# Performance work log

Measured on AMD Instinct MI355X. Metric: run time of the kernel, lower is better.

## Reference

```python
import jax, jax.numpy as jnp
import numpy as np
from jax import lax

B, T, F, H, D = 16384, 79, 3, 256, 256  # batch, levels, n_input_fields, rnn_channels, dense_width


def setup_inputs() -> dict:
    key = jax.random.key(0)
    ks = jax.random.split(key, 8)
    return {
        "x0": jax.random.normal(ks[0], (B, T), dtype=jnp.float32),
        "x1": jax.random.normal(ks[1], (B, T), dtype=jnp.float32),
        "x2": jax.random.normal(ks[2], (B, T), dtype=jnp.float32),
        # SimpleRNN params: kernel [F,H], recurrent kernel [H,H] (scaled small so relu recurrence stays stable), bias [H]
        "W_in": jax.random.normal(ks[3], (F, H), dtype=jnp.float32) * 0.1,
        "U": jax.random.normal(ks[4], (H, H), dtype=jnp.float32) * 0.05,
        "b_rnn": jnp.zeros((H,), dtype=jnp.float32),
        # MLPBlock depth=1: single Dense(D)
        "W_d": jax.random.normal(ks[5], (H, D), dtype=jnp.float32) * 0.05,
        "b_d": jnp.zeros((D,), dtype=jnp.float32),
    }


def reference(x0, x1, x2, W_in, U, b_rnn, W_d, b_d):
    # CombineInputs(-1, expand=True): stack fields on new trailing axis -> [B, T, F]
    x = jnp.stack([x0, x1, x2], axis=-1)
    # go_backwards=True: SimpleRNN consumes the sequence in reverse order
    x = x[:, ::-1, :]
    # Batched input projection (hoisted out of the recurrence): [B, T, H]
    xp = jnp.einsum("btf,fh->bth", x, W_in) + b_rnn
    xp_t = jnp.swapaxes(xp, 0, 1)  # [T, B, H] for scan over time

    def step(h, xt):
        h = jax.nn.relu(xt + h @ U)
        return h, None

    h0 = jnp.zeros((x.shape[0], W_in.shape[1]), dtype=x.dtype)
    hT, _ = lax.scan(step, h0, xp_t)  # final hidden state [B, H]
    # MLPBlock(depth=1, combine_inputs=False): single Dense, no activation
    return hT @ W_d + b_d
```

## Files before the change

### kernel.cpp

```cpp
#include <hip/hip_runtime.h>
#include <hip/hip_bf16.h>
#include <stdint.h>

#define Bsz   16384
#define Tt    79
#define Dd    256
#define KP    272
#define LROW  280
#define NTILE 32
#define THR   256

typedef __attribute__((ext_vector_type(8)))  short short8;
typedef __attribute__((ext_vector_type(4)))  float float4_;
typedef __attribute__((ext_vector_type(16))) float float16_;

__device__ __forceinline__ unsigned short f2bf(float f){
  unsigned u = __float_as_uint(f);
  u += 0x7fffu + ((u >> 16) & 1u);
  return (unsigned short)(u >> 16);
}
__device__ __forceinline__ unsigned pk2(float a, float b){
  __hip_bfloat162 h = __float22bfloat162_rn(make_float2(a, b));
  return *(unsigned*)&h;
}

__global__ void build_tables(const float* __restrict__ W_in,
                             const float* __restrict__ U,
                             const float* __restrict__ b_rnn,
                             const float* __restrict__ W_d,
                             const float* __restrict__ b_d,
                             unsigned short* __restrict__ Ut,
                             unsigned short* __restrict__ Wdt){
  const int TBL = 256 * KP;
  int idx = blockIdx.x * 256 + threadIdx.x;
  if (idx >= 2 * TBL) return;
  int tb  = idx / TBL;
  int rem = idx - tb * TBL;
  int m = rem / KP;
  int k = rem - m * KP;
  float v = 0.f;
  if (tb == 0){
    if      (k < 256) v = U[k * 256 + m];
    else if (k < 259) v = W_in[(k - 256) * 256 + m];
    else if (k == 259) v = b_rnn[m];
  } else {
    if      (k < 256) v = W_d[k * 256 + m];
    else if (k == 259) v = b_d[m];
  }
  unsigned short o = f2bf(v);
  if (tb == 0) Ut[rem] = o; else Wdt[rem] = o;
}

__global__ __launch_bounds__(THR, 2) void rnn_main(
    const float* __restrict__ x0,
    const float* __restrict__ x1,
    const float* __restrict__ x2,
    const unsigned short* __restrict__ Ut,
    const unsigned short* __restrict__ Wdt,
    float* __restrict__ out){
  __shared__ __align__(16) short hbuf[2][NTILE * LROW];

  const int tid  = threadIdx.x;
  const int lane = tid & 63;
  const int wm   = tid >> 6;
  const int nl   = lane & 31;
  const int hi   = lane >> 5;
  const int hi8  = hi * 8;
  const int bbase = blockIdx.x * NTILE;

  {
    int4* p = (int4*)&hbuf[0][0];
    const int tot = 2 * NTILE * LROW * 2 / 16;
    int4 z = make_int4(0, 0, 0, 0);
    for (int i = tid; i < tot; i += THR) p[i] = z;
  }
  __syncthreads();

  if (tid < NTILE){
    hbuf[0][tid * LROW + 259] = (short)0x3F80;
    hbuf[1][tid * LROW + 259] = (short)0x3F80;
  }

  const bool stager = (lane < 8);
  const int  sn  = wm * 8 + (lane & 7);
  const int  sgb = bbase + sn;
  if (stager){
    int tr = Tt - 1;
    float a = x0[sgb * Tt + tr];
    float b = x1[sgb * Tt + tr];
    float c = x2[sgb * Tt + tr];
    *(unsigned*)&hbuf[0][sn * LROW + 256] = pk2(a, b);
    hbuf[0][sn * LROW + 258] = (short)f2bf(c);
  }

  short8 afr[2][17];
  #pragma unroll
  for (int mt = 0; mt < 2; ++mt){
    const unsigned short* p = Ut + (wm * 64 + mt * 32 + nl) * KP + hi8;
    #pragma unroll
    for (int kt = 0; kt < 17; ++kt){
      afr[mt][kt] = *(const short8*)(p + kt * 16);
    }
  }

  __syncthreads();

  const float16_ zz16 = {0.f,0.f,0.f,0.f,0.f,0.f,0.f,0.f,
                         0.f,0.f,0.f,0.f,0.f,0.f,0.f,0.f};

  auto step = [&](const short* __restrict__ hb, short* __restrict__ hw, int t){
    float xa = 0.f, xb = 0.f, xc = 0.f;
    const bool pf = stager && (t < Tt - 1);
    if (pf){
      int tr = Tt - 2 - t;
      xa = x0[sgb * Tt + tr];
      xb = x1[sgb * Tt + tr];
      xc = x2[sgb * Tt + tr];
    }

    float16_ a0, a1;
    #pragma unroll
    for (int kt = 0; kt < 17; ++kt){
      short8 b = *(const short8*)&hb[nl * LROW + kt * 16 + hi8];
      if (kt == 0){
        a0 = __builtin_amdgcn_mfma_f32_32x32x16_bf16(afr[0][0], b, zz16, 0, 0, 0);
        a1 = __builtin_amdgcn_mfma_f32_32x32x16_bf16(afr[1][0], b, zz16, 0, 0, 0);
      } else {
        a0 = __builtin_amdgcn_mfma_f32_32x32x16_bf16(afr[0][kt], b, a0, 0, 0, 0);
        a1 = __builtin_amdgcn_mfma_f32_32x32x16_bf16(afr[1][kt], b, a1, 0, 0, 0);
      }
    }

    #pragma unroll
    for (int g = 0; g < 4; ++g){
      uint2 w;
      w.x = pk2(fmaxf(a0[4*g+0], 0.f), fmaxf(a0[4*g+1], 0.f));
      w.y = pk2(fmaxf(a0[4*g+2], 0.f), fmaxf(a0[4*g+3], 0.f));
      *(uint2*)&hw[nl * LROW + wm * 64 +      8 * g + 4 * hi] = w;
      w.x = pk2(fmaxf(a1[4*g+0], 0.f), fmaxf(a1[4*g+1], 0.f));
      w.y = pk2(fmaxf(a1[4*g+2], 0.f), fmaxf(a1[4*g+3], 0.f));
      *(uint2*)&hw[nl * LROW + wm * 64 + 32 + 8 * g + 4 * hi] = w;
    }
    if (pf){
      *(unsigned*)&hw[sn * LROW + 256] = pk2(xa, xb);
      hw[sn * LROW + 258] = (short)f2bf(xc);
    }
    __syncthreads();
  };

  #pragma unroll 1
  for (int t = 0; t < Tt - 1; t += 2){
    step(&hbuf[0][0], &hbuf[1][0], t);
    step(&hbuf[1][0], &hbuf[0][0], t + 1);
  }
  step(&hbuf[0][0], &hbuf[1][0], Tt - 1);

  const short* hb = &hbuf[1][0];
  float16_ o0, o1;
  #pragma unroll
  for (int kt = 0; kt < 17; ++kt){
    short8 w0 = *(const short8*)(Wdt + (wm * 64 +      nl) * KP + kt * 16 + hi8);
    short8 w1 = *(const short8*)(Wdt + (wm * 64 + 32 + nl) * KP + kt * 16 + hi8);
    short8 b  = *(const short8*)&hb[nl * LROW + kt * 16 + hi8];
    if (kt == 0){
      o0 = __builtin_amdgcn_mfma_f32_32x32x16_bf16(w0, b, zz16, 0, 0, 0);
      o1 = __builtin_amdgcn_mfma_f32_32x32x16_bf16(w1, b, zz16, 0, 0, 0);
    } else {
      o0 = __builtin_amdgcn_mfma_f32_32x32x16_bf16(w0, b, o0, 0, 0, 0);
      o1 = __builtin_amdgcn_mfma_f32_32x32x16_bf16(w1, b, o1, 0, 0, 0);
    }
  }
  #pragma unroll
  for (int g = 0; g < 4; ++g){
    int m0 = wm * 64 + 8 * g + 4 * hi;
    float4_ v0 = {o0[4*g+0], o0[4*g+1], o0[4*g+2], o0[4*g+3]};
    float4_ v1 = {o1[4*g+0], o1[4*g+1], o1[4*g+2], o1[4*g+3]};
    *(float4_*)&out[(bbase + nl) * Dd + m0]      = v0;
    *(float4_*)&out[(bbase + nl) * Dd + m0 + 32] = v1;
  }
}

extern "C" void kernel_launch(void* const* d_in, const int* in_sizes, int n_in,
                              void* d_out, int out_size, void* d_ws, size_t ws_size,
                              hipStream_t stream){
  const float* x0    = (const float*)d_in[0];
  const float* x1    = (const float*)d_in[1];
  const float* x2    = (const float*)d_in[2];
  const float* W_in  = (const float*)d_in[3];
  const float* U     = (const float*)d_in[4];
  const float* b_rnn = (const float*)d_in[5];
  const float* W_d   = (const float*)d_in[6];
  const float* b_d   = (const float*)d_in[7];

  unsigned short* Ut  = (unsigned short*)d_ws;
  unsigned short* Wdt = Ut + 256 * KP;
  float* out = (float*)d_out;

  build_tables<<<(2 * 256 * KP + 255) / 256, 256, 0, stream>>>(W_in, U, b_rnn, W_d, b_d, Ut, Wdt);
  rnn_main<<<Bsz / NTILE, THR, 0, stream>>>(x0, x1, x2, Ut, Wdt, out);
}
```

Measured before the change: 223.2 us.

## Fuse weight table build into RNN kernel and split hidden dim across 8 waves

Drops the separate table-building kernel: each wave now loads U, W_in, b_rnn, W_d and b_d straight from fp32 global memory and packs them to bf16 in registers. The block grows to 512 threads, so each of 8 waves owns 32 hidden channels instead of 64. That halves the MFMA chain per wave per timestep and the register-resident weight fragments, and the launch bound now asks for 4 blocks per CU to raise occupancy. The costs are strided uncoalesced fp32 weight loads repeated by every block, and a barrier each timestep that now spans twice as many waves.

```diff
diff --git a/kernel.cpp b/kernel.cpp
--- a/kernel.cpp
+++ b/kernel.cpp
@@ -8,55 +8,31 @@
 #define KP    272
 #define LROW  280
 #define NTILE 32
-#define THR   256
+#define THR   512
 
 typedef __attribute__((ext_vector_type(8)))  short short8;
 typedef __attribute__((ext_vector_type(4)))  float float4_;
 typedef __attribute__((ext_vector_type(16))) float float16_;
 
+__device__ __forceinline__ unsigned pk2(float a, float b){
+  __hip_bfloat162 h = __float22bfloat162_rn(make_float2(a, b));
+  return *(unsigned*)&h;
+}
 __device__ __forceinline__ unsigned short f2bf(float f){
   unsigned u = __float_as_uint(f);
   u += 0x7fffu + ((u >> 16) & 1u);
   return (unsigned short)(u >> 16);
 }
-__device__ __forceinline__ unsigned pk2(float a, float b){
-  __hip_bfloat162 h = __float22bfloat162_rn(make_float2(a, b));
-  return *(unsigned*)&h;
-}
 
-__global__ void build_tables(const float* __restrict__ W_in,
-                             const float* __restrict__ U,
-                             const float* __restrict__ b_rnn,
-                             const float* __restrict__ W_d,
-                             const float* __restrict__ b_d,
-                             unsigned short* __restrict__ Ut,
-                             unsigned short* __restrict__ Wdt){
-  const int TBL = 256 * KP;
-  int idx = blockIdx.x * 256 + threadIdx.x;
-  if (idx >= 2 * TBL) return;
-  int tb  = idx / TBL;
-  int rem = idx - tb * TBL;
-  int m = rem / KP;
-  int k = rem - m * KP;
-  float v = 0.f;
-  if (tb == 0){
-    if      (k < 256) v = U[k * 256 + m];
-    else if (k < 259) v = W_in[(k - 256) * 256 + m];
-    else if (k == 259) v = b_rnn[m];
-  } else {
-    if      (k < 256) v = W_d[k * 256 + m];
-    else if (k == 259) v = b_d[m];
-  }
-  unsigned short o = f2bf(v);
-  if (tb == 0) Ut[rem] = o; else Wdt[rem] = o;
-}
-
-__global__ __launch_bounds__(THR, 2) void rnn_main(
+__global__ __launch_bounds__(THR, 4) void rnn_all(
     const float* __restrict__ x0,
     const float* __restrict__ x1,
     const float* __restrict__ x2,
-    const unsigned short* __restrict__ Ut,
-    const unsigned short* __restrict__ Wdt,
+    const float* __restrict__ W_in,
+    const float* __restrict__ U,
+    const float* __restrict__ b_rnn,
+    const float* __restrict__ W_d,
+    const float* __restrict__ b_d,
     float* __restrict__ out){
   __shared__ __align__(16) short hbuf[2][NTILE * LROW];
 
@@ -67,6 +43,7 @@
   const int hi   = lane >> 5;
   const int hi8  = hi * 8;
   const int bbase = blockIdx.x * NTILE;
+  const int mcol  = wm * 32 + nl;
 
   {
     int4* p = (int4*)&hbuf[0][0];
@@ -81,8 +58,8 @@
     hbuf[1][tid * LROW + 259] = (short)0x3F80;
   }
 
-  const bool stager = (lane < 8);
-  const int  sn  = wm * 8 + (lane & 7);
+  const bool stager = (lane < 4);
+  const int  sn  = wm * 4 + (lane & 3);
   const int  sgb = bbase + sn;
   if (stager){
     int tr = Tt - 1;
@@ -93,14 +70,28 @@
     hbuf[0][sn * LROW + 258] = (short)f2bf(c);
   }
 
-  short8 afr[2][17];
+  short8 afr[17];
   #pragma unroll
-  for (int mt = 0; mt < 2; ++mt){
-    const unsigned short* p = Ut + (wm * 64 + mt * 32 + nl) * KP + hi8;
+  for (int kt = 0; kt < 16; ++kt){
+    float f[8];
     #pragma unroll
-    for (int kt = 0; kt < 17; ++kt){
-      afr[mt][kt] = *(const short8*)(p + kt * 16);
+    for (int j = 0; j < 8; ++j)
+      f[j] = U[(kt * 16 + hi8 + j) * 256 + mcol];
+    union { unsigned u[4]; short8 s; } r;
+    r.u[0] = pk2(f[0], f[1]); r.u[1] = pk2(f[2], f[3]);
+    r.u[2] = pk2(f[4], f[5]); r.u[3] = pk2(f[6], f[7]);
+    afr[kt] = r.s;
+  }
+  {
+    union { unsigned u[4]; short8 s; } r;
+    if (hi == 0){
+      r.u[0] = pk2(W_in[0 * 256 + mcol], W_in[1 * 256 + mcol]);
+      r.u[1] = pk2(W_in[2 * 256 + mcol], b_rnn[mcol]);
+      r.u[2] = 0; r.u[3] = 0;
+    } else {
+      r.u[0] = 0; r.u[1] = 0; r.u[2] = 0; r.u[3] = 0;
     }
+    afr[16] = r.s;
   }
 
   __syncthreads();
@@ -118,28 +109,22 @@
       xc = x2[sgb * Tt + tr];
     }
 
-    float16_ a0, a1;
+    float16_ a0;
+    const short* bbase_p = &hb[nl * LROW + hi8];
     #pragma unroll
     for (int kt = 0; kt < 17; ++kt){
-      short8 b = *(const short8*)&hb[nl * LROW + kt * 16 + hi8];
-      if (kt == 0){
-        a0 = __builtin_amdgcn_mfma_f32_32x32x16_bf16(afr[0][0], b, zz16, 0, 0, 0);
-        a1 = __builtin_amdgcn_mfma_f32_32x32x16_bf16(afr[1][0], b, zz16, 0, 0, 0);
-      } else {
-        a0 = __builtin_amdgcn_mfma_f32_32x32x16_bf16(afr[0][kt], b, a0, 0, 0, 0);
-        a1 = __builtin_amdgcn_mfma_f32_32x32x16_bf16(afr[1][kt], b, a1, 0, 0, 0);
-      }
+      short8 b = *(const short8*)(bbase_p + kt * 16);
+      a0 = __builtin_amdgcn_mfma_f32_32x32x16_bf16(afr[kt], b,
+                                                   kt ? a0 : zz16, 0, 0, 0);
     }
 
+    short* wr = &hw[nl * LROW + wm * 32 + 4 * hi];
     #pragma unroll
     for (int g = 0; g < 4; ++g){
       uint2 w;
       w.x = pk2(fmaxf(a0[4*g+0], 0.f), fmaxf(a0[4*g+1], 0.f));
       w.y = pk2(fmaxf(a0[4*g+2], 0.f), fmaxf(a0[4*g+3], 0.f));
-      *(uint2*)&hw[nl * LROW + wm * 64 +      8 * g + 4 * hi] = w;
-      w.x = pk2(fmaxf(a1[4*g+0], 0.f), fmaxf(a1[4*g+1], 0.f));
-      w.y = pk2(fmaxf(a1[4*g+2], 0.f), fmaxf(a1[4*g+3], 0.f));
-      *(uint2*)&hw[nl * LROW + wm * 64 + 32 + 8 * g + 4 * hi] = w;
+      *(uint2*)(wr + 8 * g) = w;
     }
     if (pf){
       *(unsigned*)&hw[sn * LROW + 256] = pk2(xa, xb);
@@ -156,27 +141,28 @@
   step(&hbuf[0][0], &hbuf[1][0], Tt - 1);
 
   const short* hb = &hbuf[1][0];
-  float16_ o0, o1;
+  float16_ o0;
   #pragma unroll
   for (int kt = 0; kt < 17; ++kt){
-    short8 w0 = *(const short8*)(Wdt + (wm * 64 +      nl) * KP + kt * 16 + hi8);
-    short8 w1 = *(const short8*)(Wdt + (wm * 64 + 32 + nl) * KP + kt * 16 + hi8);
-    short8 b  = *(const short8*)&hb[nl * LROW + kt * 16 + hi8];
-    if (kt == 0){
-      o0 = __builtin_amdgcn_mfma_f32_32x32x16_bf16(w0, b, zz16, 0, 0, 0);
-      o1 = __builtin_amdgcn_mfma_f32_32x32x16_bf16(w1, b, zz16, 0, 0, 0);
+    union { unsigned u[4]; short8 s; } r;
+    if (kt < 16){
+      float f[8];
+      #pragma unroll
+      for (int j = 0; j < 8; ++j)
+        f[j] = W_d[(kt * 16 + hi8 + j) * 256 + mcol];
+      r.u[0] = pk2(f[0], f[1]); r.u[1] = pk2(f[2], f[3]);
+      r.u[2] = pk2(f[4], f[5]); r.u[3] = pk2(f[6], f[7]);
     } else {
-      o0 = __builtin_amdgcn_mfma_f32_32x32x16_bf16(w0, b, o0, 0, 0, 0);
-      o1 = __builtin_amdgcn_mfma_f32_32x32x16_bf16(w1, b, o1, 0, 0, 0);
+      if (hi == 0){ r.u[0] = 0; r.u[1] = pk2(0.f, b_d[mcol]); r.u[2] = 0; r.u[3] = 0; }
+      else        { r.u[0] = 0; r.u[1] = 0;                   r.u[2] = 0; r.u[3] = 0; }
     }
+    short8 b = *(const short8*)&hb[nl * LROW + kt * 16 + hi8];
+    o0 = __builtin_amdgcn_mfma_f32_32x32x16_bf16(r.s, b, kt ? o0 : zz16, 0, 0, 0);
   }
   #pragma unroll
   for (int g = 0; g < 4; ++g){
-    int m0 = wm * 64 + 8 * g + 4 * hi;
-    float4_ v0 = {o0[4*g+0], o0[4*g+1], o0[4*g+2], o0[4*g+3]};
-    float4_ v1 = {o1[4*g+0], o1[4*g+1], o1[4*g+2], o1[4*g+3]};
-    *(float4_*)&out[(bbase + nl) * Dd + m0]      = v0;
-    *(float4_*)&out[(bbase + nl) * Dd + m0 + 32] = v1;
+    float4_ v = {o0[4*g+0], o0[4*g+1], o0[4*g+2], o0[4*g+3]};
+    *(float4_*)&out[(bbase + nl) * Dd + wm * 32 + 8 * g + 4 * hi] = v;
   }
 }
 
@@ -191,11 +177,7 @@
   const float* b_rnn = (const float*)d_in[5];
   const float* W_d   = (const float*)d_in[6];
   const float* b_d   = (const float*)d_in[7];
-
-  unsigned short* Ut  = (unsigned short*)d_ws;
-  unsigned short* Wdt = Ut + 256 * KP;
   float* out = (float*)d_out;
 
-  build_tables<<<(2 * 256 * KP + 255) / 256, 256, 0, stream>>>(W_in, U, b_rnn, W_d, b_d, Ut, Wdt);
-  rnn_main<<<Bsz / NTILE, THR, 0, stream>>>(x0, x1, x2, Ut, Wdt, out);
+  rnn_all<<<Bsz / NTILE, THR, 0, stream>>>(x0, x1, x2, W_in, U, b_rnn, W_d, b_d, out);
 }
```

New measurement: 282.6 us. 26.6% more time.
